# Kernel tuning notes

Hardware: AMD Instinct MI355X
Metric: run time of the kernel (lower is better)

## Reference

```python
import jax, jax.numpy as jnp
import numpy as np

N_HEADS = 8  # from init_kwargs


def setup_inputs() -> dict:
    key = jax.random.key(0)
    ks = jax.random.split(key, 12)
    P, B, V, F = 12, 32, 32, 256          # len_pred, batch, n_vehicles, feature_size
    S, NL, LF = 32, 16, 64                # lane_size, n_lanes, lane_feature_size
    T = 20                                # obs horizon for mask_input
    inp = {
        "query": jax.random.normal(ks[0], (P, B, V, F), jnp.float32),
        "lanes": jax.random.normal(ks[1], (S, B, NL, LF), jnp.float32),
        "mask_input": jax.random.bernoulli(ks[2], 0.8, (T, B, V)),
        "mask_lanes": jax.random.bernoulli(ks[3], 0.8, (S, B, NL)),
        # nn.Linear params stored as (in, out) so y = x @ W + b
        "Wk": jax.random.normal(ks[4], (LF, F), jnp.float32) * 0.05,
        "bk": jax.random.normal(ks[5], (F,), jnp.float32) * 0.05,
        "Wv": jax.random.normal(ks[6], (LF, F), jnp.float32) * 0.05,
        "bv": jax.random.normal(ks[7], (F,), jnp.float32) * 0.05,
        "Wc": jax.random.normal(ks[8], (F, F), jnp.float32) * 0.05,
        "bc": jax.random.normal(ks[9], (F,), jnp.float32) * 0.05,
    }
    return inp


def reference(query, lanes, mask_input, mask_lanes, Wk, bk, Wv, bv, Wc, bc):
    P, B, V, F = query.shape
    S, _, NL, LF = lanes.shape
    H = N_HEADS
    d = F // H
    L = NL * S

    # lanes: (S,B,NL,LF) -> (B, NL*S, LF)  [lane-major flatten, as in torch]
    lanes_f = lanes.transpose(1, 2, 0, 3).reshape(B, L, LF)
    key = (lanes_f @ Wk + bk).reshape(B, L, H, d).transpose(0, 2, 1, 3)    # (B,H,L,d)
    value = (lanes_f @ Wv + bv).reshape(B, L, H, d).transpose(0, 2, 1, 3)  # (B,H,L,d)

    # mask_lanes: (S,B,NL) -> (B, S*NL)  [position-major flatten, as in torch]
    ml = mask_lanes[:S].transpose(1, 0, 2).reshape(B, S * NL)
    mi = jnp.any(mask_input, axis=0)              # (B,V): valid at any obs step
    mask = ml[:, None, :] & mi[:, :, None]        # (B,V,L)

    q = query.reshape(P, B, V, H, d).transpose(0, 1, 3, 2, 4)  # (P,B,H,V,d)

    # scale=1 in the original call -> no 1/sqrt(d_k) division
    scores = jnp.einsum('pbhvd,bhld->pbhvl', q, key)           # (P,B,H,V,L)
    scores = jnp.where(mask[None, :, None, :, :], scores, -1e9)
    p_attn = jax.nn.softmax(scores, axis=-1)

    # geometric aggregation: exp(P @ log(sigmoid(V)))
    out = jnp.exp(jnp.einsum('pbhvl,bhld->pbhvd', p_attn, jax.nn.log_sigmoid(value)))
    out = out.transpose(0, 1, 3, 2, 4).reshape(P, B, V, F)
    return out @ Wc + bc  # attention_combine (n_heads > 1)
```

## Files before the change

### kernel.cpp

```cpp
#include <hip/hip_runtime.h>
#include <cstdint>

#define P_ 12
#define B_ 32
#define V_ 32
#define F_ 256
#define S_ 32
#define NL_ 16
#define LF_ 64
#define T_ 20
#define H_ 8
#define D_ 32
#define L_ 512

typedef short bf16x8 __attribute__((ext_vector_type(8)));
typedef short bf16x4 __attribute__((ext_vector_type(4)));
typedef float f32x4 __attribute__((ext_vector_type(4)));

static __device__ __forceinline__ short f2bf(float f) {
  uint32_t u = __builtin_bit_cast(uint32_t, f);
  uint32_t r = u + 0x7FFFu + ((u >> 16) & 1u);
  return (short)(r >> 16);
}

static __device__ __forceinline__ uint32_t cvtpk(float lo, float hi) {
  uint32_t r;
  asm("v_cvt_pk_bf16_f32 %0, %1, %2" : "=v"(r) : "v"(lo), "v"(hi));
  return r;
}
static __device__ __forceinline__ bf16x8 pack8(uint32_t d0, uint32_t d1,
                                               uint32_t d2, uint32_t d3) {
  uint4 u = {d0, d1, d2, d3};
  return __builtin_bit_cast(bf16x8, u);
}
static __device__ __forceinline__ bf16x4 pack4(uint32_t d0, uint32_t d1) {
  uint2 u = {d0, d1};
  return __builtin_bit_cast(bf16x4, u);
}
static __device__ __forceinline__ float vexp2(float x) {
  float y;
  asm("v_exp_f32 %0, %1" : "=v"(y) : "v"(x));
  return y;
}
static __device__ __forceinline__ float vlog2(float x) {
  float y;
  asm("v_log_f32 %0, %1" : "=v"(y) : "v"(x));
  return y;
}

#define L2E 1.4426950408889634f
#define LN2 0.6931471805599453f

__global__ __launch_bounds__(256) void prep_kernel(
    const float* __restrict__ Wk, const float* __restrict__ Wv,
    const float* __restrict__ Wc,
    const int* __restrict__ mask_input, const int* __restrict__ mask_lanes,
    short* __restrict__ WkT, short* __restrict__ WvT, short* __restrict__ WcT,
    unsigned int* __restrict__ maskr, int* __restrict__ mi) {
  int t = blockIdx.x * 256 + threadIdx.x;
  if (t < 2048) {
    int f = t >> 3, k0 = (t & 7) * 8;
    bf16x8 o;
#pragma unroll
    for (int e = 0; e < 8; ++e) o[e] = f2bf(Wk[(k0 + e) * F_ + f]);
    *(bf16x8*)&WkT[f * LF_ + k0] = o;
  } else if (t < 4096) {
    int i = t - 2048;
    int f = i >> 3, k0 = (i & 7) * 8;
    bf16x8 o;
#pragma unroll
    for (int e = 0; e < 8; ++e) o[e] = f2bf(Wv[(k0 + e) * F_ + f]);
    *(bf16x8*)&WvT[f * LF_ + k0] = o;
  } else if (t < 12288) {
    int i = t - 4096;
    int f = i >> 5, k0 = (i & 31) * 8;
    bf16x8 o;
#pragma unroll
    for (int e = 0; e < 8; ++e) o[e] = f2bf(Wc[(k0 + e) * F_ + f]);
    *(bf16x8*)&WcT[f * F_ + k0] = o;
  } else if (t < 12800) {
    int i = t - 12288;
    int b = i >> 4, r = i & 15;
    unsigned int bits = 0u;
    for (int lt = 0; lt < 32; ++lt)
      if (mask_lanes[(lt * B_ + b) * NL_ + r]) bits |= (1u << lt);
    maskr[i] = bits;
  } else if (t < 13824) {
    int i = t - 12800;
    int b = i >> 5, v = i & 31;
    int any = 0;
    for (int tt = 0; tt < T_; ++tt) any |= mask_input[(tt * B_ + b) * V_ + v];
    mi[i] = any ? 1 : 0;
  }
}

__global__ __launch_bounds__(512, 2) void attn_kernel(
    const float* __restrict__ query, const float* __restrict__ lanes,
    const short* __restrict__ WkT, const short* __restrict__ WvT,
    const float* __restrict__ bk, const float* __restrict__ bv,
    const unsigned int* __restrict__ maskr, const int* __restrict__ mi,
    short* __restrict__ out0b) {
  __shared__ short Ks[512 * 40];
  __shared__ short Vt[32 * 520];

  int i0 = blockIdx.x;
  int xcd = i0 & 7, widx = i0 >> 3;
  int b = xcd * 4 + widx / 24;
  int rem = widx % 24;
  int h = rem & 7, pg = rem >> 3;

  int tid = threadIdx.x;
  int w = tid >> 6, lane = tid & 63;
  int r = lane & 15, g = lane >> 4;
  const f32x4 zero = {0.f, 0.f, 0.f, 0.f};

  {
    bf16x8 wk[2][2], wv[2][2];
#pragma unroll
    for (int dt = 0; dt < 2; ++dt)
#pragma unroll
      for (int c = 0; c < 2; ++c) {
        int f = h * 32 + dt * 16 + r;
        wk[dt][c] = *(const bf16x8*)&WkT[f * LF_ + c * 32 + g * 8];
        wv[dt][c] = *(const bf16x8*)&WvT[f * LF_ + c * 32 + g * 8];
      }
    float4 bk4[2];
    float bvf[2];
#pragma unroll
    for (int dt = 0; dt < 2; ++dt) {
      bk4[dt] = *(const float4*)&bk[h * 32 + dt * 16 + g * 4];
      bvf[dt] = bv[h * 32 + dt * 16 + r];
    }

#pragma unroll
    for (int lt = 0; lt < 4; ++lt) {
      int l0 = w * 64 + lt * 16;
      int l = l0 + r;
      int nl = l >> 5, s = l & 31;
      const float* xrow = &lanes[((s * B_ + b) * NL_ + nl) * LF_];
      bf16x8 xf[2];
#pragma unroll
      for (int c = 0; c < 2; ++c) {
        float4 a = *(const float4*)&xrow[c * 32 + g * 8];
        float4 q = *(const float4*)&xrow[c * 32 + g * 8 + 4];
        xf[c] = pack8(cvtpk(a.x, a.y), cvtpk(a.z, a.w),
                      cvtpk(q.x, q.y), cvtpk(q.z, q.w));
      }
      int sl = (l & ~31) | (((l >> 2) & 1) << 4) | (((l >> 3) & 3) << 2) | (l & 3);
#pragma unroll
      for (int dt = 0; dt < 2; ++dt) {
        f32x4 aK = __builtin_amdgcn_mfma_f32_16x16x32_bf16(wk[dt][0], xf[0], zero, 0, 0, 0);
        aK = __builtin_amdgcn_mfma_f32_16x16x32_bf16(wk[dt][1], xf[1], aK, 0, 0, 0);
        *(bf16x4*)&Ks[sl * 40 + dt * 16 + g * 4] =
            pack4(cvtpk(aK[0] + bk4[dt].x, aK[1] + bk4[dt].y),
                  cvtpk(aK[2] + bk4[dt].z, aK[3] + bk4[dt].w));
        f32x4 aV = __builtin_amdgcn_mfma_f32_16x16x32_bf16(xf[0], wv[dt][0], zero, 0, 0, 0);
        aV = __builtin_amdgcn_mfma_f32_16x16x32_bf16(xf[1], wv[dt][1], aV, 0, 0, 0);
        float ls[4];
#pragma unroll
        for (int reg = 0; reg < 4; ++reg) {
          float x = aV[reg] + bvf[dt];
          float z = vexp2(fabsf(x) * -L2E);
          ls[reg] = fminf(x, 0.f) - vlog2(1.f + z) * LN2;
        }
        *(bf16x4*)&Vt[(dt * 16 + r) * 520 + l0 + g * 4] =
            pack4(cvtpk(ls[0], ls[1]), cvtpk(ls[2], ls[3]));
      }
    }
  }

  int band = pg * 8 + w;
  int p = band >> 1, vb = (band & 1) << 4;
  const float* qp = &query[((p * B_ + b) * V_ + vb + r) * F_ + h * D_ + g * 8];
  float4 qa = *(const float4*)qp;
  float4 qq = *(const float4*)(qp + 4);
  bf16x8 qf = pack8(cvtpk(qa.x, qa.y), cvtpk(qa.z, qa.w),
                    cvtpk(qq.x, qq.y), cvtpk(qq.z, qq.w));
  float hiB = mi[b * V_ + vb + r] ? (-40.f * L2E) : -1.44269504e9f;
  const float loB = -1.44269504e9f;

  unsigned int mw[8];
#pragma unroll
  for (int q8 = 0; q8 < 8; ++q8) mw[q8] = maskr[b * 16 + ((g & 1) << 3) + q8];
  int ghalf = g >> 1;

  float rsum = 0.f;
  f32x4 O0 = zero, O1 = zero;

  __syncthreads();

  for (int ch = 0; ch < 4; ++ch) {
    bf16x8 Kf[8];
#pragma unroll
    for (int t = 0; t < 8; ++t)
      Kf[t] = *(const bf16x8*)&Ks[((ch * 8 + t) * 16 + r) * 40 + g * 8];

    bf16x8 vbuf[4][2];
#pragma unroll
    for (int ks = 0; ks < 4; ++ks) {
      vbuf[ks][0] = *(const bf16x8*)&Vt[r * 520 + ch * 128 + ks * 32 + g * 8];
      vbuf[ks][1] = *(const bf16x8*)&Vt[(16 + r) * 520 + ch * 128 + ks * 32 + g * 8];
    }

    f32x4 sc[8];
#pragma unroll
    for (int t = 0; t < 8; ++t)
      sc[t] = __builtin_amdgcn_mfma_f32_16x16x32_bf16(Kf[t], qf, zero, 0, 0, 0);

#pragma unroll
    for (int ks = 0; ks < 4; ++ks) {
      int bitidx = ch * 8 + 2 * ks + ghalf;
      float f0 = ((mw[0] >> bitidx) & 1u) ? hiB : loB;
      float f1 = ((mw[1] >> bitidx) & 1u) ? hiB : loB;
      float f2 = ((mw[2] >> bitidx) & 1u) ? hiB : loB;
      float f3 = ((mw[3] >> bitidx) & 1u) ? hiB : loB;
      float f4 = ((mw[4] >> bitidx) & 1u) ? hiB : loB;
      float f5 = ((mw[5] >> bitidx) & 1u) ? hiB : loB;
      float f6 = ((mw[6] >> bitidx) & 1u) ? hiB : loB;
      float f7 = ((mw[7] >> bitidx) & 1u) ? hiB : loB;
      float p0 = vexp2(fmaf(sc[2 * ks][0], L2E, f0));
      float p1 = vexp2(fmaf(sc[2 * ks][1], L2E, f1));
      float p2 = vexp2(fmaf(sc[2 * ks][2], L2E, f2));
      float p3 = vexp2(fmaf(sc[2 * ks][3], L2E, f3));
      float p4 = vexp2(fmaf(sc[2 * ks + 1][0], L2E, f4));
      float p5 = vexp2(fmaf(sc[2 * ks + 1][1], L2E, f5));
      float p6 = vexp2(fmaf(sc[2 * ks + 1][2], L2E, f6));
      float p7 = vexp2(fmaf(sc[2 * ks + 1][3], L2E, f7));
      rsum += ((p0 + p1) + (p2 + p3)) + ((p4 + p5) + (p6 + p7));
      bf16x8 pa = pack8(cvtpk(p0, p1), cvtpk(p2, p3),
                        cvtpk(p4, p5), cvtpk(p6, p7));
      O0 = __builtin_amdgcn_mfma_f32_16x16x32_bf16(pa, vbuf[ks][0], O0, 0, 0, 0);
      O1 = __builtin_amdgcn_mfma_f32_16x16x32_bf16(pa, vbuf[ks][1], O1, 0, 0, 0);
    }
  }

  float rs = rsum;
  rs += __shfl_xor(rs, 16);
  rs += __shfl_xor(rs, 32);
  float invv = rs > 0.f ? 1.f / rs : 0.f;
#pragma unroll
  for (int j = 0; j < 4; ++j) {
    float inv = __shfl(invv, g * 4 + j);
    int v = vb + g * 4 + j;
    short* op = &out0b[(((h * P_ + p) * B_ + b) * V_ + v) * D_];
    op[r] = f2bf(__expf(O0[j] * inv));
    op[16 + r] = f2bf(__expf(O1[j] * inv));
  }
}

__global__ __launch_bounds__(256) void combine_kernel(
    const short* __restrict__ out0b, const short* __restrict__ WcT,
    const float* __restrict__ bc, float* __restrict__ out) {
  int blk = blockIdx.x;
  int xcd = blk & 7;
  int r3 = blk >> 3;
  int pgrp = r3 >> 3;
  int bblsb = (r3 >> 2) & 1;
  int ftq = r3 & 3;
  int bb = xcd * 2 + bblsb;
  int rblk = pgrp * 16 + bb;
  int tid = threadIdx.x;
  int w = tid >> 6, lane = tid & 63;
  int r = lane & 15, g = lane >> 4;
  int R = rblk * 64 + w * 16;

  bf16x8 xf[8];
#pragma unroll
  for (int c = 0; c < 8; ++c)
    xf[c] = *(const bf16x8*)&out0b[(c * (P_ * B_ * V_) + R + r) * D_ + g * 8];

  const f32x4 zero = {0.f, 0.f, 0.f, 0.f};
#pragma unroll
  for (int fi = 0; fi < 4; ++fi) {
    int ft = ftq * 4 + fi;
    f32x4 acc = zero;
#pragma unroll
    for (int c = 0; c < 8; ++c) {
      bf16x8 wf = *(const bf16x8*)&WcT[(ft * 16 + r) * F_ + c * 32 + g * 8];
      acc = __builtin_amdgcn_mfma_f32_16x16x32_bf16(wf, xf[c], acc, 0, 0, 0);
    }
    float4 bc4 = *(const float4*)&bc[ft * 16 + g * 4];
    float4 o;
    o.x = acc[0] + bc4.x;
    o.y = acc[1] + bc4.y;
    o.z = acc[2] + bc4.z;
    o.w = acc[3] + bc4.w;
    *(float4*)&out[(R + r) * F_ + ft * 16 + g * 4] = o;
  }
}

extern "C" void kernel_launch(void* const* d_in, const int* in_sizes, int n_in,
                              void* d_out, int out_size, void* d_ws, size_t ws_size,
                              hipStream_t stream) {
  const float* query = (const float*)d_in[0];
  const float* lanes = (const float*)d_in[1];
  const int* mask_input = (const int*)d_in[2];
  const int* mask_lanes = (const int*)d_in[3];
  const float* Wk = (const float*)d_in[4];
  const float* bk = (const float*)d_in[5];
  const float* Wv = (const float*)d_in[6];
  const float* bv = (const float*)d_in[7];
  const float* Wc = (const float*)d_in[8];
  const float* bc = (const float*)d_in[9];
  float* out = (float*)d_out;

  char* wp = (char*)d_ws;
  short* out0b = (short*)wp; wp += 6291456;
  short* WkT = (short*)wp;   wp += 32768;
  short* WvT = (short*)wp;   wp += 32768;
  short* WcT = (short*)wp;   wp += 131072;
  unsigned int* maskr = (unsigned int*)wp; wp += 2048;
  int* mi = (int*)wp;        wp += 4096;

  prep_kernel<<<54, 256, 0, stream>>>(Wk, Wv, Wc, mask_input, mask_lanes,
                                      WkT, WvT, WcT, maskr, mi);
  attn_kernel<<<B_ * H_ * 3, 512, 0, stream>>>(query, lanes, WkT, WvT, bk, bv,
                                               maskr, mi, out0b);
  combine_kernel<<<768, 256, 0, stream>>>(out0b, WcT, bc, out);
}
```

Before: 53.80 us.

## Stage K/V projections in two halves to halve LDS footprint

Splits the lane dimension into two 256-long chunks. Each chunk is projected into shared memory, consumed by the attention loop, then overwritten by the next chunk, with barriers in between. This halves the LDS allocation so more blocks can be resident per CU. In exchange it adds two extra barriers and serializes the second projection after the first half of attention.

```diff
diff --git a/kernel.cpp b/kernel.cpp
--- a/kernel.cpp
+++ b/kernel.cpp
@@ -94,14 +94,102 @@
   }
 }
 
+#define STAGE_CHUNK(CCH)                                                      \
+  {                                                                           \
+    bf16x8 wk[2][2], wv[2][2];                                                \
+    _Pragma("unroll") for (int dt = 0; dt < 2; ++dt)                          \
+        _Pragma("unroll") for (int c = 0; c < 2; ++c) {                       \
+      int f = h * 32 + dt * 16 + r;                                           \
+      wk[dt][c] = *(const bf16x8*)&WkT[f * LF_ + c * 32 + g * 8];             \
+      wv[dt][c] = *(const bf16x8*)&WvT[f * LF_ + c * 32 + g * 8];             \
+    }                                                                         \
+    _Pragma("unroll") for (int lt = 0; lt < 2; ++lt) {                        \
+      int l0c = w * 32 + lt * 16;                                             \
+      int l = (CCH)*256 + l0c + r;                                            \
+      int nl = l >> 5, s = l & 31;                                            \
+      const float* xrow = &lanes[((s * B_ + b) * NL_ + nl) * LF_];            \
+      bf16x8 xf[2];                                                           \
+      _Pragma("unroll") for (int c = 0; c < 2; ++c) {                         \
+        float4 a = *(const float4*)&xrow[c * 32 + g * 8];                     \
+        float4 q = *(const float4*)&xrow[c * 32 + g * 8 + 4];                 \
+        xf[c] = pack8(cvtpk(a.x, a.y), cvtpk(a.z, a.w),                       \
+                      cvtpk(q.x, q.y), cvtpk(q.z, q.w));                      \
+      }                                                                       \
+      int ll = l0c + r;                                                       \
+      int slc = (ll & ~31) | (((ll >> 2) & 1) << 4) |                         \
+                (((ll >> 3) & 3) << 2) | (ll & 3);                            \
+      _Pragma("unroll") for (int dt = 0; dt < 2; ++dt) {                      \
+        f32x4 aK = __builtin_amdgcn_mfma_f32_16x16x32_bf16(wk[dt][0], xf[0],  \
+                                                           zero, 0, 0, 0);    \
+        aK = __builtin_amdgcn_mfma_f32_16x16x32_bf16(wk[dt][1], xf[1], aK, 0, \
+                                                     0, 0);                   \
+        *(bf16x4*)&Ks[slc * 40 + dt * 16 + g * 4] =                           \
+            pack4(cvtpk(aK[0] + bk4[dt].x, aK[1] + bk4[dt].y),                \
+                  cvtpk(aK[2] + bk4[dt].z, aK[3] + bk4[dt].w));               \
+        f32x4 aV = __builtin_amdgcn_mfma_f32_16x16x32_bf16(xf[0], wv[dt][0],  \
+                                                           zero, 0, 0, 0);    \
+        aV = __builtin_amdgcn_mfma_f32_16x16x32_bf16(xf[1], wv[dt][1], aV, 0, \
+                                                     0, 0);                   \
+        float ls[4];                                                          \
+        _Pragma("unroll") for (int reg = 0; reg < 4; ++reg) {                 \
+          float x = aV[reg] + bvf[dt];                                        \
+          float z = vexp2(fabsf(x) * -L2E);                                   \
+          ls[reg] = fminf(x, 0.f) - vlog2(1.f + z) * LN2;                     \
+        }                                                                     \
+        *(bf16x4*)&Vt[(dt * 16 + r) * 264 + l0c + g * 4] =                    \
+            pack4(cvtpk(ls[0], ls[1]), cvtpk(ls[2], ls[3]));                  \
+      }                                                                       \
+    }                                                                         \
+  }
+
+#define COMPUTE_CHUNK(CHH, CH)                                                \
+  {                                                                           \
+    bf16x8 Kf[8];                                                             \
+    _Pragma("unroll") for (int t = 0; t < 8; ++t) Kf[t] =                     \
+        *(const bf16x8*)&Ks[(((CHH)*8 + t) * 16 + r) * 40 + g * 8];           \
+    bf16x8 vb0[4], vb1[4];                                                    \
+    _Pragma("unroll") for (int ks = 0; ks < 4; ++ks) {                        \
+      vb0[ks] = *(const bf16x8*)&Vt[r * 264 + (CHH)*128 + ks * 32 + g * 8];   \
+      vb1[ks] =                                                               \
+          *(const bf16x8*)&Vt[(16 + r) * 264 + (CHH)*128 + ks * 32 + g * 8];  \
+    }                                                                         \
+    f32x4 sc[8];                                                              \
+    _Pragma("unroll") for (int t = 0; t < 8; ++t) sc[t] =                     \
+        __builtin_amdgcn_mfma_f32_16x16x32_bf16(Kf[t], qf, zero, 0, 0, 0);    \
+    _Pragma("unroll") for (int ks = 0; ks < 4; ++ks) {                        \
+      int bitidx = (CH)*8 + 2 * ks + ghalf;                                   \
+      float f0 = ((mw[0] >> bitidx) & 1u) ? hiB : loB;                        \
+      float f1 = ((mw[1] >> bitidx) & 1u) ? hiB : loB;                        \
+      float f2 = ((mw[2] >> bitidx) & 1u) ? hiB : loB;                        \
+      float f3 = ((mw[3] >> bitidx) & 1u) ? hiB : loB;                        \
+      float f4 = ((mw[4] >> bitidx) & 1u) ? hiB : loB;                        \
+      float f5 = ((mw[5] >> bitidx) & 1u) ? hiB : loB;                        \
+      float f6 = ((mw[6] >> bitidx) & 1u) ? hiB : loB;                        \
+      float f7 = ((mw[7] >> bitidx) & 1u) ? hiB : loB;                        \
+      float p0 = vexp2(fmaf(sc[2 * ks][0], L2E, f0));                         \
+      float p1 = vexp2(fmaf(sc[2 * ks][1], L2E, f1));                         \
+      float p2 = vexp2(fmaf(sc[2 * ks][2], L2E, f2));                         \
+      float p3 = vexp2(fmaf(sc[2 * ks][3], L2E, f3));                         \
+      float p4 = vexp2(fmaf(sc[2 * ks + 1][0], L2E, f4));                     \
+      float p5 = vexp2(fmaf(sc[2 * ks + 1][1], L2E, f5));                     \
+      float p6 = vexp2(fmaf(sc[2 * ks + 1][2], L2E, f6));                     \
+      float p7 = vexp2(fmaf(sc[2 * ks + 1][3], L2E, f7));                     \
+      rsum += ((p0 + p1) + (p2 + p3)) + ((p4 + p5) + (p6 + p7));              \
+      bf16x8 pa =                                                             \
+          pack8(cvtpk(p0, p1), cvtpk(p2, p3), cvtpk(p4, p5), cvtpk(p6, p7));  \
+      O0 = __builtin_amdgcn_mfma_f32_16x16x32_bf16(pa, vb0[ks], O0, 0, 0, 0); \
+      O1 = __builtin_amdgcn_mfma_f32_16x16x32_bf16(pa, vb1[ks], O1, 0, 0, 0); \
+    }                                                                         \
+  }
+
 __global__ __launch_bounds__(512, 2) void attn_kernel(
     const float* __restrict__ query, const float* __restrict__ lanes,
     const short* __restrict__ WkT, const short* __restrict__ WvT,
     const float* __restrict__ bk, const float* __restrict__ bv,
     const unsigned int* __restrict__ maskr, const int* __restrict__ mi,
     short* __restrict__ out0b) {
-  __shared__ short Ks[512 * 40];
-  __shared__ short Vt[32 * 520];
+  __shared__ short Ks[256 * 40];
+  __shared__ short Vt[32 * 264];
 
   int i0 = blockIdx.x;
   int xcd = i0 & 7, widx = i0 >> 3;
@@ -114,60 +202,15 @@
   int r = lane & 15, g = lane >> 4;
   const f32x4 zero = {0.f, 0.f, 0.f, 0.f};
 
-  {
-    bf16x8 wk[2][2], wv[2][2];
-#pragma unroll
-    for (int dt = 0; dt < 2; ++dt)
-#pragma unroll
-      for (int c = 0; c < 2; ++c) {
-        int f = h * 32 + dt * 16 + r;
-        wk[dt][c] = *(const bf16x8*)&WkT[f * LF_ + c * 32 + g * 8];
-        wv[dt][c] = *(const bf16x8*)&WvT[f * LF_ + c * 32 + g * 8];
-      }
-    float4 bk4[2];
-    float bvf[2];
-#pragma unroll
-    for (int dt = 0; dt < 2; ++dt) {
-      bk4[dt] = *(const float4*)&bk[h * 32 + dt * 16 + g * 4];
-      bvf[dt] = bv[h * 32 + dt * 16 + r];
-    }
-
-#pragma unroll
-    for (int lt = 0; lt < 4; ++lt) {
-      int l0 = w * 64 + lt * 16;
-      int l = l0 + r;
-      int nl = l >> 5, s = l & 31;
-      const float* xrow = &lanes[((s * B_ + b) * NL_ + nl) * LF_];
-      bf16x8 xf[2];
-#pragma unroll
-      for (int c = 0; c < 2; ++c) {
-        float4 a = *(const float4*)&xrow[c * 32 + g * 8];
-        float4 q = *(const float4*)&xrow[c * 32 + g * 8 + 4];
-        xf[c] = pack8(cvtpk(a.x, a.y), cvtpk(a.z, a.w),
-                      cvtpk(q.x, q.y), cvtpk(q.z, q.w));
-      }
-      int sl = (l & ~31) | (((l >> 2) & 1) << 4) | (((l >> 3) & 3) << 2) | (l & 3);
-#pragma unroll
-      for (int dt = 0; dt < 2; ++dt) {
-        f32x4 aK = __builtin_amdgcn_mfma_f32_16x16x32_bf16(wk[dt][0], xf[0], zero, 0, 0, 0);
-        aK = __builtin_amdgcn_mfma_f32_16x16x32_bf16(wk[dt][1], xf[1], aK, 0, 0, 0);
-        *(bf16x4*)&Ks[sl * 40 + dt * 16 + g * 4] =
-            pack4(cvtpk(aK[0] + bk4[dt].x, aK[1] + bk4[dt].y),
-                  cvtpk(aK[2] + bk4[dt].z, aK[3] + bk4[dt].w));
-        f32x4 aV = __builtin_amdgcn_mfma_f32_16x16x32_bf16(xf[0], wv[dt][0], zero, 0, 0, 0);
-        aV = __builtin_amdgcn_mfma_f32_16x16x32_bf16(xf[1], wv[dt][1], aV, 0, 0, 0);
-        float ls[4];
-#pragma unroll
-        for (int reg = 0; reg < 4; ++reg) {
-          float x = aV[reg] + bvf[dt];
-          float z = vexp2(fabsf(x) * -L2E);
-          ls[reg] = fminf(x, 0.f) - vlog2(1.f + z) * LN2;
-        }
-        *(bf16x4*)&Vt[(dt * 16 + r) * 520 + l0 + g * 4] =
-            pack4(cvtpk(ls[0], ls[1]), cvtpk(ls[2], ls[3]));
-      }
-    }
-  }
+  float4 bk4[2];
+  float bvf[2];
+#pragma unroll
+  for (int dt = 0; dt < 2; ++dt) {
+    bk4[dt] = *(const float4*)&bk[h * 32 + dt * 16 + g * 4];
+    bvf[dt] = bv[h * 32 + dt * 16 + r];
+  }
+
+  STAGE_CHUNK(0)
 
   int band = pg * 8 + w;
   int p = band >> 1, vb = (band & 1) << 4;
@@ -188,51 +231,13 @@
   f32x4 O0 = zero, O1 = zero;
 
   __syncthreads();
-
-  for (int ch = 0; ch < 4; ++ch) {
-    bf16x8 Kf[8];
-#pragma unroll
-    for (int t = 0; t < 8; ++t)
-      Kf[t] = *(const bf16x8*)&Ks[((ch * 8 + t) * 16 + r) * 40 + g * 8];
-
-    bf16x8 vbuf[4][2];
-#pragma unroll
-    for (int ks = 0; ks < 4; ++ks) {
-      vbuf[ks][0] = *(const bf16x8*)&Vt[r * 520 + ch * 128 + ks * 32 + g * 8];
-      vbuf[ks][1] = *(const bf16x8*)&Vt[(16 + r) * 520 + ch * 128 + ks * 32 + g * 8];
-    }
-
-    f32x4 sc[8];
-#pragma unroll
-    for (int t = 0; t < 8; ++t)
-      sc[t] = __builtin_amdgcn_mfma_f32_16x16x32_bf16(Kf[t], qf, zero, 0, 0, 0);
-
-#pragma unroll
-    for (int ks = 0; ks < 4; ++ks) {
-      int bitidx = ch * 8 + 2 * ks + ghalf;
-      float f0 = ((mw[0] >> bitidx) & 1u) ? hiB : loB;
-      float f1 = ((mw[1] >> bitidx) & 1u) ? hiB : loB;
-      float f2 = ((mw[2] >> bitidx) & 1u) ? hiB : loB;
-      float f3 = ((mw[3] >> bitidx) & 1u) ? hiB : loB;
-      float f4 = ((mw[4] >> bitidx) & 1u) ? hiB : loB;
-      float f5 = ((mw[5] >> bitidx) & 1u) ? hiB : loB;
-      float f6 = ((mw[6] >> bitidx) & 1u) ? hiB : loB;
-      float f7 = ((mw[7] >> bitidx) & 1u) ? hiB : loB;
-      float p0 = vexp2(fmaf(sc[2 * ks][0], L2E, f0));
-      float p1 = vexp2(fmaf(sc[2 * ks][1], L2E, f1));
-      float p2 = vexp2(fmaf(sc[2 * ks][2], L2E, f2));
-      float p3 = vexp2(fmaf(sc[2 * ks][3], L2E, f3));
-      float p4 = vexp2(fmaf(sc[2 * ks + 1][0], L2E, f4));
-      float p5 = vexp2(fmaf(sc[2 * ks + 1][1], L2E, f5));
-      float p6 = vexp2(fmaf(sc[2 * ks + 1][2], L2E, f6));
-      float p7 = vexp2(fmaf(sc[2 * ks + 1][3], L2E, f7));
-      rsum += ((p0 + p1) + (p2 + p3)) + ((p4 + p5) + (p6 + p7));
-      bf16x8 pa = pack8(cvtpk(p0, p1), cvtpk(p2, p3),
-                        cvtpk(p4, p5), cvtpk(p6, p7));
-      O0 = __builtin_amdgcn_mfma_f32_16x16x32_bf16(pa, vbuf[ks][0], O0, 0, 0, 0);
-      O1 = __builtin_amdgcn_mfma_f32_16x16x32_bf16(pa, vbuf[ks][1], O1, 0, 0, 0);
-    }
-  }
+  COMPUTE_CHUNK(0, 0)
+  COMPUTE_CHUNK(1, 1)
+  __syncthreads();
+  STAGE_CHUNK(1)
+  __syncthreads();
+  COMPUTE_CHUNK(0, 2)
+  COMPUTE_CHUNK(1, 3)
 
   float rs = rsum;
   rs += __shfl_xor(rs, 16);
```

Measured after the change: 63.87 us. 18.7% more time.
